# Performance work log

Hardware: AMD Instinct MI355X
Metric: run time of the kernel (lower is better)

Reference implementation:

```python
import jax, jax.numpy as jnp
import numpy as np

N, K = 10000, 32          # nodes, max neighbors
NUM_ELEM = 100
D_ATOM = 128              # atom embedding size
D_DIR_IN, D_DIR = 10, 64  # node direction expansion -> embedding
D_DIST_IN, D_DIST = 128, 128  # edge distance expansion -> embedding


def setup_inputs() -> dict:
    key = jax.random.key(0)
    ks = jax.random.split(key, 12)
    inp = {
        "atomic_numbers": jax.random.randint(ks[0], (N,), 0, NUM_ELEM),
        "node_direction_expansion": jax.random.normal(ks[1], (N, D_DIR_IN), jnp.float32),
        "edge_distance_expansion": jax.random.normal(ks[2], (N, K, D_DIST_IN), jnp.float32),
        "neighbor_list": jax.random.randint(ks[3], (N, K), 0, N),
        "neighbor_mask": jax.random.randint(ks[4], (N, K), 0, 2).astype(bool),
        # learned params
        "src_atom_emb": jax.random.uniform(ks[5], (NUM_ELEM, D_ATOM), jnp.float32, -0.001, 0.001),
        "tgt_atom_emb": jax.random.uniform(ks[6], (NUM_ELEM, D_ATOM), jnp.float32, -0.001, 0.001),
        "src_dir_W": jax.random.normal(ks[7], (D_DIR_IN, D_DIR), jnp.float32) * 0.1,
        "src_dir_b": jnp.zeros((D_DIR,), jnp.float32),
        "tgt_dir_W": jax.random.normal(ks[8], (D_DIR_IN, D_DIR), jnp.float32) * 0.1,
        "tgt_dir_b": jnp.zeros((D_DIR,), jnp.float32),
        "dist_W": jax.random.normal(ks[9], (D_DIST_IN, D_DIST), jnp.float32) * 0.1,
        "dist_b": jnp.zeros((D_DIST,), jnp.float32),
    }
    return inp


def reference(atomic_numbers, node_direction_expansion, edge_distance_expansion,
              neighbor_list, neighbor_mask,
              src_atom_emb, tgt_atom_emb,
              src_dir_W, src_dir_b, tgt_dir_W, tgt_dir_b, dist_W, dist_b):
    # per-node embeddings
    sa = src_atom_emb[atomic_numbers]                      # [N, D_ATOM]
    ta = tgt_atom_emb[atomic_numbers]                      # [N, D_ATOM]
    sd = jax.nn.silu(node_direction_expansion @ src_dir_W + src_dir_b)  # [N, D_DIR]
    td = jax.nn.silu(node_direction_expansion @ tgt_dir_W + tgt_dir_b)  # [N, D_DIR]

    # map_sender_receiver_feature: sender gathered via neighbor_list, receiver broadcast
    sender_atom = sa[neighbor_list]                        # [N, K, D_ATOM]
    recv_atom = jnp.broadcast_to(ta[:, None, :], (N, K, D_ATOM))
    sender_dir = sd[neighbor_list]                         # [N, K, D_DIR]
    recv_dir = jnp.broadcast_to(td[:, None, :], (N, K, D_DIR))

    edist = jax.nn.silu(edge_distance_expansion @ dist_W + dist_b)  # [N, K, D_DIST]

    edge_features = jnp.concatenate(
        [edist, sender_dir, sender_atom, recv_dir, recv_atom], axis=-1)  # [N, K, 512]

    # masked mean over neighbors
    m = neighbor_mask.astype(edge_features.dtype)          # [N, K]
    count = m.sum(axis=1, keepdims=True) + 1e-5            # [N, 1]
    out = (edge_features * m[:, :, None]).sum(axis=1) / count  # [N, 512]
    return out
```

## Files before the change

kernel.cpp:

```cpp
#include <hip/hip_runtime.h>
#include <hip/hip_bf16.h>

#define NN 10000
#define KK 32
#define DDIRIN 10
#define DDIR 64
#define DD 128

typedef short bf16x8 __attribute__((ext_vector_type(8)));
typedef float f32x4  __attribute__((ext_vector_type(4)));

__device__ __forceinline__ float silu_f(float x) { return x / (1.0f + __expf(-x)); }

__device__ __forceinline__ ushort2 pk_bf16(float a, float b) {
    __hip_bfloat162 h = __float22bfloat162_rn(float2{a, b});
    union { __hip_bfloat162 h; ushort2 u; } v; v.h = h;
    return v.u;
}

__global__ __launch_bounds__(256) void dir_kernel(
    const float* __restrict__ nde,
    const float* __restrict__ sW, const float* __restrict__ sb,
    const float* __restrict__ tW, const float* __restrict__ tb,
    float* __restrict__ sd, float* __restrict__ td)
{
    int gid = blockIdx.x * 256 + threadIdx.x;
    if (gid >= NN * DDIR) return;
    int n = gid >> 6, d = gid & 63;
    float a = sb[d], t = tb[d];
    const float* x = nde + n * DDIRIN;
#pragma unroll
    for (int i = 0; i < DDIRIN; ++i) {
        float xv = x[i];
        a = fmaf(xv, sW[i * DDIR + d], a);
        t = fmaf(xv, tW[i * DDIR + d], t);
    }
    sd[gid] = silu_f(a);
    td[gid] = silu_f(t);
}

__global__ __launch_bounds__(256, 2) void gemm_kernel(
    const float* __restrict__ edist,
    const int*   __restrict__ nmask,
    const float* __restrict__ dW,
    const float* __restrict__ db,
    float* __restrict__ out)
{
    const int tid  = threadIdx.x;
    const int wid  = tid >> 6;
    const int lane = tid & 63;
    const int l15  = lane & 15;
    const int quad = lane >> 4;
    const int n0   = blockIdx.x * 4;

    __shared__ __align__(16) short s_E[128 * 128];
    __shared__ float s_cnt[4];

    bf16x8 bfrag[2][4];
    float  bias[2];
#pragma unroll
    for (int c2 = 0; c2 < 2; ++c2) {
        int ncol = (2 * wid + c2) * 16 + l15;
        bias[c2] = db[ncol];
#pragma unroll
        for (int t = 0; t < 4; ++t) {
            bf16x8 v;
#pragma unroll
            for (int j2 = 0; j2 < 4; ++j2) {
                int k0 = t * 32 + quad * 8 + 2 * j2;
                ushort2 u = pk_bf16(dW[k0 * DD + ncol], dW[(k0 + 1) * DD + ncol]);
                v[2 * j2]     = (short)u.x;
                v[2 * j2 + 1] = (short)u.y;
            }
            bfrag[c2][t] = v;
        }
    }

    {
        const float4* E4 = reinterpret_cast<const float4*>(edist + (size_t)n0 * (KK * DD));
        const int* nm = nmask + n0 * KK;
#pragma unroll
        for (int i = 0; i < 8; ++i) {
            int f0  = 2 * tid + 512 * i;
            int row = f0 >> 5;
            float4 a = E4[f0], b = E4[f0 + 1];
            ushort2 u0 = pk_bf16(a.x, a.y), u1 = pk_bf16(a.z, a.w);
            ushort2 u2 = pk_bf16(b.x, b.y), u3 = pk_bf16(b.z, b.w);
            bf16x8 v;
            v[0] = (short)u0.x; v[1] = (short)u0.y; v[2] = (short)u1.x; v[3] = (short)u1.y;
            v[4] = (short)u2.x; v[5] = (short)u2.y; v[6] = (short)u3.x; v[7] = (short)u3.y;
            bf16x8 z; 
#pragma unroll
            for (int q = 0; q < 8; ++q) z[q] = 0;
            v = (nm[row] != 0) ? v : z;
            int kb = tid & 15;
            int sw = kb ^ (row & 7);
            *reinterpret_cast<bf16x8*>(&s_E[row * 128 + sw * 8]) = v;
        }
        if (tid < 4) {
            int c = 0;
#pragma unroll 8
            for (int k = 0; k < KK; ++k) c += (nm[tid * KK + k] != 0) ? 1 : 0;
            s_cnt[tid] = (float)c;
        }
    }
    __syncthreads();

    f32x4 acc[8][2];
#pragma unroll
    for (int rt = 0; rt < 8; ++rt)
#pragma unroll
        for (int c2 = 0; c2 < 2; ++c2)
#pragma unroll
            for (int g = 0; g < 4; ++g) acc[rt][c2][g] = 0.0f;

#pragma unroll
    for (int rt = 0; rt < 8; ++rt) {
        bf16x8 af[4];
        int r = rt * 16 + l15;
#pragma unroll
        for (int t = 0; t < 4; ++t) {
            int kb = (4 * t + quad) ^ (l15 & 7);
            af[t] = *reinterpret_cast<const bf16x8*>(&s_E[r * 128 + kb * 8]);
        }
#pragma unroll
        for (int t = 0; t < 4; ++t) {
            acc[rt][0] = __builtin_amdgcn_mfma_f32_16x16x32_bf16(af[t], bfrag[0][t], acc[rt][0], 0, 0, 0);
            acc[rt][1] = __builtin_amdgcn_mfma_f32_16x16x32_bf16(af[t], bfrag[1][t], acc[rt][1], 0, 0, 0);
        }
    }

#pragma unroll
    for (int c2 = 0; c2 < 2; ++c2) {
        float sbv = silu_f(bias[c2]);
#pragma unroll
        for (int nd = 0; nd < 4; ++nd) {
            float p = 0.0f;
#pragma unroll
            for (int h = 0; h < 2; ++h) {
                int rt = 2 * nd + h;
#pragma unroll
                for (int g = 0; g < 4; ++g)
                    p += silu_f(acc[rt][c2][g] + bias[c2]);
            }
            p += __shfl_xor(p, 16);
            p += __shfl_xor(p, 32);
            if (quad == nd) {
                float c = s_cnt[nd];
                float val = (p - (32.0f - c) * sbv) / (c + 1e-5f);
                out[(size_t)(n0 + nd) * 512 + (2 * wid + c2) * 16 + l15] = val;
            }
        }
    }
}

template<bool USE_WS>
__global__ __launch_bounds__(256) void seg_kernel(
    const int*   __restrict__ an,
    const float* __restrict__ nde,
    const int*   __restrict__ nl,
    const int*   __restrict__ nmask,
    const float* __restrict__ semb,
    const float* __restrict__ temb,
    const float* __restrict__ sW, const float* __restrict__ sb,
    const float* __restrict__ tW, const float* __restrict__ tb,
    const float* __restrict__ sd_ws,
    const float* __restrict__ td_ws,
    float* __restrict__ out)
{
    const int tid  = threadIdx.x;
    const int wid  = tid >> 6;
    const int lane = tid & 63;
    const int n    = blockIdx.x * 4 + wid;

    __shared__ int s_idx[4][KK];
    __shared__ int s_aidx[4][KK];

    int j = 0; bool act = false;
    if (lane < KK) {
        j   = nl[n * KK + lane];
        act = (nmask[n * KK + lane] != 0);
    }
    unsigned long long bits = __ballot(act);
    int cnt = (int)__popcll(bits);
    if (act) {
        int rank = (int)__popcll(bits & ((1ull << lane) - 1ull));
        s_idx[wid][rank]  = j;
        s_aidx[wid][rank] = an[j];
    }
    __syncthreads();

    const float invv  = 1.0f / ((float)cnt + 1e-5f);
    const float scale = (float)cnt * invv;
    float* outn = out + (size_t)n * 512;

    {
        float s = 0.0f;
        if constexpr (USE_WS) {
#pragma unroll 4
            for (int i = 0; i < cnt; ++i)
                s += sd_ws[s_idx[wid][i] * DDIR + lane];
        } else {
            for (int i = 0; i < cnt; ++i) {
                int jj = s_idx[wid][i];
                float a = sb[lane];
#pragma unroll
                for (int q = 0; q < DDIRIN; ++q)
                    a = fmaf(nde[jj * DDIRIN + q], sW[q * DDIR + lane], a);
                s += silu_f(a);
            }
        }
        outn[128 + lane] = s * invv;
    }

    {
        float s0 = 0.0f, s1 = 0.0f;
#pragma unroll 4
        for (int i = 0; i < cnt; ++i) {
            int a = s_aidx[wid][i];
            s0 += semb[a * DD + lane];
            s1 += semb[a * DD + 64 + lane];
        }
        outn[192 + lane] = s0 * invv;
        outn[256 + lane] = s1 * invv;
    }

    {
        float tdv;
        if constexpr (USE_WS) {
            tdv = td_ws[n * DDIR + lane];
        } else {
            float a = tb[lane];
#pragma unroll
            for (int q = 0; q < DDIRIN; ++q)
                a = fmaf(nde[n * DDIRIN + q], tW[q * DDIR + lane], a);
            tdv = silu_f(a);
        }
        outn[320 + lane] = tdv * scale;
    }

    {
        int ann = an[n];
        outn[384 + lane] = temb[ann * DD + lane] * scale;
        outn[448 + lane] = temb[ann * DD + 64 + lane] * scale;
    }
}

extern "C" void kernel_launch(void* const* d_in, const int* in_sizes, int n_in,
                              void* d_out, int out_size, void* d_ws, size_t ws_size,
                              hipStream_t stream) {
    const int*   an    = (const int*)  d_in[0];
    const float* nde   = (const float*)d_in[1];
    const float* edist = (const float*)d_in[2];
    const int*   nl    = (const int*)  d_in[3];
    const int*   nmask = (const int*)  d_in[4];
    const float* semb  = (const float*)d_in[5];
    const float* temb  = (const float*)d_in[6];
    const float* sW    = (const float*)d_in[7];
    const float* sb    = (const float*)d_in[8];
    const float* tW    = (const float*)d_in[9];
    const float* tb    = (const float*)d_in[10];
    const float* dW    = (const float*)d_in[11];
    const float* db    = (const float*)d_in[12];
    float* out = (float*)d_out;

    gemm_kernel<<<NN / 4, 256, 0, stream>>>(edist, nmask, dW, db, out);

    const size_t need = (size_t)NN * DDIR * sizeof(float) * 2;
    if (ws_size >= need) {
        float* sd = (float*)d_ws;
        float* td = sd + (size_t)NN * DDIR;
        dir_kernel<<<(NN * DDIR + 255) / 256, 256, 0, stream>>>(nde, sW, sb, tW, tb, sd, td);
        seg_kernel<true><<<NN / 4, 256, 0, stream>>>(
            an, nde, nl, nmask, semb, temb, sW, sb, tW, tb, sd, td, out);
    } else {
        seg_kernel<false><<<NN / 4, 256, 0, stream>>>(
            an, nde, nl, nmask, semb, temb, sW, sb, tW, tb, nullptr, nullptr, out);
    }
}
```

Measured before the change: 281.6 us.

## Fuse direction, segment-sum and distance GEMM kernels into one launch

```diff
diff --git a/kernel.cpp b/kernel.cpp
--- a/kernel.cpp
+++ b/kernel.cpp
@@ -9,6 +9,7 @@
 
 typedef short bf16x8 __attribute__((ext_vector_type(8)));
 typedef float f32x4  __attribute__((ext_vector_type(4)));
+typedef float f32x2  __attribute__((ext_vector_type(2)));
 
 __device__ __forceinline__ float silu_f(float x) { return x / (1.0f + __expf(-x)); }
 
@@ -18,30 +19,16 @@
     return v.u;
 }
 
-__global__ __launch_bounds__(256) void dir_kernel(
+__global__ __launch_bounds__(256, 2) void fused_kernel(
+    const int*   __restrict__ an,
     const float* __restrict__ nde,
+    const float* __restrict__ edist,
+    const int*   __restrict__ nl,
+    const int*   __restrict__ nmask,
+    const float* __restrict__ semb,
+    const float* __restrict__ temb,
     const float* __restrict__ sW, const float* __restrict__ sb,
     const float* __restrict__ tW, const float* __restrict__ tb,
-    float* __restrict__ sd, float* __restrict__ td)
-{
-    int gid = blockIdx.x * 256 + threadIdx.x;
-    if (gid >= NN * DDIR) return;
-    int n = gid >> 6, d = gid & 63;
-    float a = sb[d], t = tb[d];
-    const float* x = nde + n * DDIRIN;
-#pragma unroll
-    for (int i = 0; i < DDIRIN; ++i) {
-        float xv = x[i];
-        a = fmaf(xv, sW[i * DDIR + d], a);
-        t = fmaf(xv, tW[i * DDIR + d], t);
-    }
-    sd[gid] = silu_f(a);
-    td[gid] = silu_f(t);
-}
-
-__global__ __launch_bounds__(256, 2) void gemm_kernel(
-    const float* __restrict__ edist,
-    const int*   __restrict__ nmask,
     const float* __restrict__ dW,
     const float* __restrict__ db,
     float* __restrict__ out)
@@ -52,9 +39,20 @@
     const int l15  = lane & 15;
     const int quad = lane >> 4;
     const int n0   = blockIdx.x * 4;
+    const int n    = n0 + wid;
 
     __shared__ __align__(16) short s_E[128 * 128];
     __shared__ float s_cnt[4];
+
+    int j = 0, aj = 0; bool act = false;
+    if (lane < KK) {
+        j   = nl[n * KK + lane];
+        act = (nmask[n * KK + lane] != 0);
+    }
+    unsigned long long bits = __ballot(act);
+    int cnt = (int)__popcll(bits);
+    if (act) aj = an[j];
+    if (lane == 0) s_cnt[wid] = (float)cnt;
 
     bf16x8 bfrag[2][4];
     float  bias[2];
@@ -77,19 +75,20 @@
     }
 
     {
-        const float4* E4 = reinterpret_cast<const float4*>(edist + (size_t)n0 * (KK * DD));
+        const f32x4* E4 = reinterpret_cast<const f32x4*>(edist + (size_t)n0 * (KK * DD));
         const int* nm = nmask + n0 * KK;
 #pragma unroll
         for (int i = 0; i < 8; ++i) {
             int f0  = 2 * tid + 512 * i;
             int row = f0 >> 5;
-            float4 a = E4[f0], b = E4[f0 + 1];
-            ushort2 u0 = pk_bf16(a.x, a.y), u1 = pk_bf16(a.z, a.w);
-            ushort2 u2 = pk_bf16(b.x, b.y), u3 = pk_bf16(b.z, b.w);
+            f32x4 a = __builtin_nontemporal_load(&E4[f0]);
+            f32x4 b = __builtin_nontemporal_load(&E4[f0 + 1]);
+            ushort2 u0 = pk_bf16(a[0], a[1]), u1 = pk_bf16(a[2], a[3]);
+            ushort2 u2 = pk_bf16(b[0], b[1]), u3 = pk_bf16(b[2], b[3]);
             bf16x8 v;
             v[0] = (short)u0.x; v[1] = (short)u0.y; v[2] = (short)u1.x; v[3] = (short)u1.y;
             v[4] = (short)u2.x; v[5] = (short)u2.y; v[6] = (short)u3.x; v[7] = (short)u3.y;
-            bf16x8 z; 
+            bf16x8 z;
 #pragma unroll
             for (int q = 0; q < 8; ++q) z[q] = 0;
             v = (nm[row] != 0) ? v : z;
@@ -97,12 +96,6 @@
             int sw = kb ^ (row & 7);
             *reinterpret_cast<bf16x8*>(&s_E[row * 128 + sw * 8]) = v;
         }
-        if (tid < 4) {
-            int c = 0;
-#pragma unroll 8
-            for (int k = 0; k < KK; ++k) c += (nm[tid * KK + k] != 0) ? 1 : 0;
-            s_cnt[tid] = (float)c;
-        }
     }
     __syncthreads();
 
@@ -148,101 +141,62 @@
             if (quad == nd) {
                 float c = s_cnt[nd];
                 float val = (p - (32.0f - c) * sbv) / (c + 1e-5f);
-                out[(size_t)(n0 + nd) * 512 + (2 * wid + c2) * 16 + l15] = val;
-            }
-        }
-    }
-}
-
-template<bool USE_WS>
-__global__ __launch_bounds__(256) void seg_kernel(
-    const int*   __restrict__ an,
-    const float* __restrict__ nde,
-    const int*   __restrict__ nl,
-    const int*   __restrict__ nmask,
-    const float* __restrict__ semb,
-    const float* __restrict__ temb,
-    const float* __restrict__ sW, const float* __restrict__ sb,
-    const float* __restrict__ tW, const float* __restrict__ tb,
-    const float* __restrict__ sd_ws,
-    const float* __restrict__ td_ws,
-    float* __restrict__ out)
-{
-    const int tid  = threadIdx.x;
-    const int wid  = tid >> 6;
-    const int lane = tid & 63;
-    const int n    = blockIdx.x * 4 + wid;
-
-    __shared__ int s_idx[4][KK];
-    __shared__ int s_aidx[4][KK];
-
-    int j = 0; bool act = false;
-    if (lane < KK) {
-        j   = nl[n * KK + lane];
-        act = (nmask[n * KK + lane] != 0);
-    }
-    unsigned long long bits = __ballot(act);
-    int cnt = (int)__popcll(bits);
-    if (act) {
-        int rank = (int)__popcll(bits & ((1ull << lane) - 1ull));
-        s_idx[wid][rank]  = j;
-        s_aidx[wid][rank] = an[j];
-    }
-    __syncthreads();
-
-    const float invv  = 1.0f / ((float)cnt + 1e-5f);
-    const float scale = (float)cnt * invv;
-    float* outn = out + (size_t)n * 512;
+                __builtin_nontemporal_store(
+                    val, &out[(size_t)(n0 + nd) * 512 + (2 * wid + c2) * 16 + l15]);
+            }
+        }
+    }
 
     {
-        float s = 0.0f;
-        if constexpr (USE_WS) {
-#pragma unroll 4
-            for (int i = 0; i < cnt; ++i)
-                s += sd_ws[s_idx[wid][i] * DDIR + lane];
-        } else {
-            for (int i = 0; i < cnt; ++i) {
-                int jj = s_idx[wid][i];
-                float a = sb[lane];
-#pragma unroll
-                for (int q = 0; q < DDIRIN; ++q)
-                    a = fmaf(nde[jj * DDIRIN + q], sW[q * DDIR + lane], a);
-                s += silu_f(a);
-            }
-        }
-        outn[128 + lane] = s * invv;
-    }
-
-    {
-        float s0 = 0.0f, s1 = 0.0f;
-#pragma unroll 4
+        const float invv  = 1.0f / ((float)cnt + 1e-5f);
+        const float scale = (float)cnt * invv;
+        float* outn = out + (size_t)n * 512;
+
+        float sw_r[DDIRIN];
+#pragma unroll
+        for (int q = 0; q < DDIRIN; ++q) sw_r[q] = sW[q * DDIR + lane];
+        const float sbv = sb[lane];
+
+        float sdir = 0.0f, sa0 = 0.0f, sa1 = 0.0f;
+        unsigned long long rem = bits;
         for (int i = 0; i < cnt; ++i) {
-            int a = s_aidx[wid][i];
-            s0 += semb[a * DD + lane];
-            s1 += semb[a * DD + 64 + lane];
-        }
-        outn[192 + lane] = s0 * invv;
-        outn[256 + lane] = s1 * invv;
-    }
-
-    {
-        float tdv;
-        if constexpr (USE_WS) {
-            tdv = td_ws[n * DDIR + lane];
-        } else {
+            int src = __builtin_ctzll(rem); rem &= rem - 1ull;
+            int jj = __shfl(j, src);
+            int ja = __shfl(aj, src);
+            const f32x2* x2 = reinterpret_cast<const f32x2*>(nde + (size_t)jj * DDIRIN);
+            float a = sbv;
+#pragma unroll
+            for (int q = 0; q < 5; ++q) {
+                f32x2 xv = x2[q];
+                a = fmaf(xv[0], sw_r[2 * q], a);
+                a = fmaf(xv[1], sw_r[2 * q + 1], a);
+            }
+            sdir += silu_f(a);
+            f32x2 e = reinterpret_cast<const f32x2*>(semb + (size_t)ja * DD)[lane];
+            sa0 += e[0]; sa1 += e[1];
+        }
+        __builtin_nontemporal_store(sdir * invv, &outn[128 + lane]);
+        f32x2 sa = {sa0 * invv, sa1 * invv};
+        __builtin_nontemporal_store(sa, reinterpret_cast<f32x2*>(&outn[192 + 2 * lane]));
+
+        {
+            const f32x2* x2 = reinterpret_cast<const f32x2*>(nde + (size_t)n * DDIRIN);
             float a = tb[lane];
 #pragma unroll
-            for (int q = 0; q < DDIRIN; ++q)
-                a = fmaf(nde[n * DDIRIN + q], tW[q * DDIR + lane], a);
-            tdv = silu_f(a);
-        }
-        outn[320 + lane] = tdv * scale;
-    }
-
-    {
-        int ann = an[n];
-        outn[384 + lane] = temb[ann * DD + lane] * scale;
-        outn[448 + lane] = temb[ann * DD + 64 + lane] * scale;
+            for (int q = 0; q < 5; ++q) {
+                f32x2 xv = x2[q];
+                a = fmaf(xv[0], tW[(2 * q) * DDIR + lane], a);
+                a = fmaf(xv[1], tW[(2 * q + 1) * DDIR + lane], a);
+            }
+            __builtin_nontemporal_store(silu_f(a) * scale, &outn[320 + lane]);
+        }
+
+        {
+            int ann = an[n];
+            f32x2 r = reinterpret_cast<const f32x2*>(temb + (size_t)ann * DD)[lane];
+            f32x2 rv = {r[0] * scale, r[1] * scale};
+            __builtin_nontemporal_store(rv, reinterpret_cast<f32x2*>(&outn[384 + 2 * lane]));
+        }
     }
 }
 
@@ -264,17 +218,6 @@
     const float* db    = (const float*)d_in[12];
     float* out = (float*)d_out;
 
-    gemm_kernel<<<NN / 4, 256, 0, stream>>>(edist, nmask, dW, db, out);
-
-    const size_t need = (size_t)NN * DDIR * sizeof(float) * 2;
-    if (ws_size >= need) {
-        float* sd = (float*)d_ws;
-        float* td = sd + (size_t)NN * DDIR;
-        dir_kernel<<<(NN * DDIR + 255) / 256, 256, 0, stream>>>(nde, sW, sb, tW, tb, sd, td);
-        seg_kernel<true><<<NN / 4, 256, 0, stream>>>(
-            an, nde, nl, nmask, semb, temb, sW, sb, tW, tb, sd, td, out);
-    } else {
-        seg_kernel<false><<<NN / 4, 256, 0, stream>>>(
-            an, nde, nl, nmask, semb, temb, sW, sb, tW, tb, nullptr, nullptr, out);
-    }
+    fused_kernel<<<NN / 4, 256, 0, stream>>>(
+        an, nde, edist, nl, nmask, semb, temb, sW, sb, tW, tb, dW, db, out);
 }
```

Measured after the change: 288.3 us. +2.4%, slower.

## Load edge-distance fragments directly to registers and pre-convert dist weights once

Applied to the files above, without the earlier changes.

```diff
diff --git a/kernel.cpp b/kernel.cpp
--- a/kernel.cpp
+++ b/kernel.cpp
@@ -9,6 +9,7 @@
 
 typedef short bf16x8 __attribute__((ext_vector_type(8)));
 typedef float f32x4  __attribute__((ext_vector_type(4)));
+typedef float f32x2  __attribute__((ext_vector_type(2)));
 
 __device__ __forceinline__ float silu_f(float x) { return x / (1.0f + __expf(-x)); }
 
@@ -18,14 +19,23 @@
     return v.u;
 }
 
-__global__ __launch_bounds__(256) void dir_kernel(
+__global__ __launch_bounds__(256) void dirprep_kernel(
     const float* __restrict__ nde,
     const float* __restrict__ sW, const float* __restrict__ sb,
     const float* __restrict__ tW, const float* __restrict__ tb,
-    float* __restrict__ sd, float* __restrict__ td)
+    const float* __restrict__ dW,
+    float* __restrict__ sd, float* __restrict__ td, ushort* __restrict__ dWb)
 {
-    int gid = blockIdx.x * 256 + threadIdx.x;
-    if (gid >= NN * DDIR) return;
+    int b = blockIdx.x;
+    if (b < 32) {
+        int v = b * 256 + threadIdx.x;
+        int ncol = v >> 6;
+        int k0   = (v & 63) * 2;
+        ushort2 u = pk_bf16(dW[k0 * DD + ncol], dW[(k0 + 1) * DD + ncol]);
+        *reinterpret_cast<ushort2*>(&dWb[ncol * DD + k0]) = u;
+        return;
+    }
+    int gid = (b - 32) * 256 + threadIdx.x;
     int n = gid >> 6, d = gid & 63;
     float a = sb[d], t = tb[d];
     const float* x = nde + n * DDIRIN;
@@ -39,11 +49,13 @@
     td[gid] = silu_f(t);
 }
 
-__global__ __launch_bounds__(256, 2) void gemm_kernel(
+template<bool PREB>
+__global__ __launch_bounds__(256, 4) void gemm_kernel(
     const float* __restrict__ edist,
     const int*   __restrict__ nmask,
     const float* __restrict__ dW,
     const float* __restrict__ db,
+    const ushort* __restrict__ dWb,
     float* __restrict__ out)
 {
     const int tid  = threadIdx.x;
@@ -51,77 +63,68 @@
     const int lane = tid & 63;
     const int l15  = lane & 15;
     const int quad = lane >> 4;
-    const int n0   = blockIdx.x * 4;
-
-    __shared__ __align__(16) short s_E[128 * 128];
-    __shared__ float s_cnt[4];
+    const int n0   = blockIdx.x * 2;
+
+    bool act = (nmask[n0 * KK + lane] != 0);
+    unsigned long long bits = __ballot(act);
+    const float cnt0 = (float)__popcll(bits & 0xffffffffull);
+    const float cnt1 = (float)__popcll(bits >> 32);
 
     bf16x8 bfrag[2][4];
     float  bias[2];
-#pragma unroll
-    for (int c2 = 0; c2 < 2; ++c2) {
-        int ncol = (2 * wid + c2) * 16 + l15;
-        bias[c2] = db[ncol];
+    if constexpr (PREB) {
+#pragma unroll
+        for (int c2 = 0; c2 < 2; ++c2) {
+            int ncol = (2 * wid + c2) * 16 + l15;
+            bias[c2] = db[ncol];
+#pragma unroll
+            for (int t = 0; t < 4; ++t)
+                bfrag[c2][t] = *reinterpret_cast<const bf16x8*>(
+                    &dWb[ncol * DD + t * 32 + quad * 8]);
+        }
+    } else {
+#pragma unroll
+        for (int c2 = 0; c2 < 2; ++c2) {
+            int ncol = (2 * wid + c2) * 16 + l15;
+            bias[c2] = db[ncol];
+#pragma unroll
+            for (int t = 0; t < 4; ++t) {
+                bf16x8 v;
+#pragma unroll
+                for (int j2 = 0; j2 < 4; ++j2) {
+                    int k0 = t * 32 + quad * 8 + 2 * j2;
+                    ushort2 u = pk_bf16(dW[k0 * DD + ncol], dW[(k0 + 1) * DD + ncol]);
+                    v[2 * j2]     = (short)u.x;
+                    v[2 * j2 + 1] = (short)u.y;
+                }
+                bfrag[c2][t] = v;
+            }
+        }
+    }
+
+    f32x4 acc[4][2];
+#pragma unroll
+    for (int rt = 0; rt < 4; ++rt)
+#pragma unroll
+        for (int c2 = 0; c2 < 2; ++c2)
+#pragma unroll
+            for (int g = 0; g < 4; ++g) acc[rt][c2][g] = 0.0f;
+
+    const float* Ebase = edist + (size_t)n0 * (KK * DD);
+#pragma unroll
+    for (int rt = 0; rt < 4; ++rt) {
+        const float* rp = Ebase + (size_t)(rt * 16 + l15) * DD + quad * 8;
+        bf16x8 af[4];
 #pragma unroll
         for (int t = 0; t < 4; ++t) {
-            bf16x8 v;
-#pragma unroll
-            for (int j2 = 0; j2 < 4; ++j2) {
-                int k0 = t * 32 + quad * 8 + 2 * j2;
-                ushort2 u = pk_bf16(dW[k0 * DD + ncol], dW[(k0 + 1) * DD + ncol]);
-                v[2 * j2]     = (short)u.x;
-                v[2 * j2 + 1] = (short)u.y;
-            }
-            bfrag[c2][t] = v;
-        }
-    }
-
-    {
-        const float4* E4 = reinterpret_cast<const float4*>(edist + (size_t)n0 * (KK * DD));
-        const int* nm = nmask + n0 * KK;
-#pragma unroll
-        for (int i = 0; i < 8; ++i) {
-            int f0  = 2 * tid + 512 * i;
-            int row = f0 >> 5;
-            float4 a = E4[f0], b = E4[f0 + 1];
-            ushort2 u0 = pk_bf16(a.x, a.y), u1 = pk_bf16(a.z, a.w);
-            ushort2 u2 = pk_bf16(b.x, b.y), u3 = pk_bf16(b.z, b.w);
+            f32x4 a = *reinterpret_cast<const f32x4*>(rp + t * 32);
+            f32x4 b = *reinterpret_cast<const f32x4*>(rp + t * 32 + 4);
+            ushort2 u0 = pk_bf16(a[0], a[1]), u1 = pk_bf16(a[2], a[3]);
+            ushort2 u2 = pk_bf16(b[0], b[1]), u3 = pk_bf16(b[2], b[3]);
             bf16x8 v;
             v[0] = (short)u0.x; v[1] = (short)u0.y; v[2] = (short)u1.x; v[3] = (short)u1.y;
             v[4] = (short)u2.x; v[5] = (short)u2.y; v[6] = (short)u3.x; v[7] = (short)u3.y;
-            bf16x8 z; 
-#pragma unroll
-            for (int q = 0; q < 8; ++q) z[q] = 0;
-            v = (nm[row] != 0) ? v : z;
-            int kb = tid & 15;
-            int sw = kb ^ (row & 7);
-            *reinterpret_cast<bf16x8*>(&s_E[row * 128 + sw * 8]) = v;
-        }
-        if (tid < 4) {
-            int c = 0;
-#pragma unroll 8
-            for (int k = 0; k < KK; ++k) c += (nm[tid * KK + k] != 0) ? 1 : 0;
-            s_cnt[tid] = (float)c;
-        }
-    }
-    __syncthreads();
-
-    f32x4 acc[8][2];
-#pragma unroll
-    for (int rt = 0; rt < 8; ++rt)
-#pragma unroll
-        for (int c2 = 0; c2 < 2; ++c2)
-#pragma unroll
-            for (int g = 0; g < 4; ++g) acc[rt][c2][g] = 0.0f;
-
-#pragma unroll
-    for (int rt = 0; rt < 8; ++rt) {
-        bf16x8 af[4];
-        int r = rt * 16 + l15;
-#pragma unroll
-        for (int t = 0; t < 4; ++t) {
-            int kb = (4 * t + quad) ^ (l15 & 7);
-            af[t] = *reinterpret_cast<const bf16x8*>(&s_E[r * 128 + kb * 8]);
+            af[t] = v;
         }
 #pragma unroll
         for (int t = 0; t < 4; ++t) {
@@ -132,23 +135,26 @@
 
 #pragma unroll
     for (int c2 = 0; c2 < 2; ++c2) {
-        float sbv = silu_f(bias[c2]);
-#pragma unroll
-        for (int nd = 0; nd < 4; ++nd) {
+#pragma unroll
+        for (int nd = 0; nd < 2; ++nd) {
             float p = 0.0f;
 #pragma unroll
             for (int h = 0; h < 2; ++h) {
                 int rt = 2 * nd + h;
-#pragma unroll
-                for (int g = 0; g < 4; ++g)
-                    p += silu_f(acc[rt][c2][g] + bias[c2]);
+                int rbase = rt * 16 + quad * 4;
+#pragma unroll
+                for (int g = 0; g < 4; ++g) {
+                    bool on = (bits >> (rbase + g)) & 1ull;
+                    float s = silu_f(acc[rt][c2][g] + bias[c2]);
+                    p += on ? s : 0.0f;
+                }
             }
             p += __shfl_xor(p, 16);
             p += __shfl_xor(p, 32);
             if (quad == nd) {
-                float c = s_cnt[nd];
-                float val = (p - (32.0f - c) * sbv) / (c + 1e-5f);
-                out[(size_t)(n0 + nd) * 512 + (2 * wid + c2) * 16 + l15] = val;
+                float c = (nd == 0) ? cnt0 : cnt1;
+                __builtin_nontemporal_store(p / (c + 1e-5f),
+                    &out[(size_t)(n0 + nd) * 512 + (2 * wid + c2) * 16 + l15]);
             }
         }
     }
@@ -264,16 +270,20 @@
     const float* db    = (const float*)d_in[12];
     float* out = (float*)d_out;
 
-    gemm_kernel<<<NN / 4, 256, 0, stream>>>(edist, nmask, dW, db, out);
-
-    const size_t need = (size_t)NN * DDIR * sizeof(float) * 2;
+    const size_t dwb_bytes = (size_t)DD * DD * sizeof(ushort);
+    const size_t need = dwb_bytes + (size_t)NN * DDIR * sizeof(float) * 2;
+
     if (ws_size >= need) {
-        float* sd = (float*)d_ws;
-        float* td = sd + (size_t)NN * DDIR;
-        dir_kernel<<<(NN * DDIR + 255) / 256, 256, 0, stream>>>(nde, sW, sb, tW, tb, sd, td);
+        ushort* dWb = (ushort*)d_ws;
+        float*  sd  = (float*)((char*)d_ws + dwb_bytes);
+        float*  td  = sd + (size_t)NN * DDIR;
+        dirprep_kernel<<<32 + NN * DDIR / 256, 256, 0, stream>>>(
+            nde, sW, sb, tW, tb, dW, sd, td, dWb);
+        gemm_kernel<true><<<NN / 2, 256, 0, stream>>>(edist, nmask, dW, db, dWb, out);
         seg_kernel<true><<<NN / 4, 256, 0, stream>>>(
             an, nde, nl, nmask, semb, temb, sW, sb, tW, tb, sd, td, out);
     } else {
+        gemm_kernel<false><<<NN / 2, 256, 0, stream>>>(edist, nmask, dW, db, nullptr, out);
         seg_kernel<false><<<NN / 4, 256, 0, stream>>>(
             an, nde, nl, nmask, semb, temb, sW, sb, tW, tb, nullptr, nullptr, out);
     }
```

Result: slower. 323.4 us (+14.9%).
